# Kernel optimization log

Measured on AMD Instinct MI355X. Metric: run time of the kernel, lower is better.

## Reference

```python
import jax, jax.numpy as jnp
import numpy as np

B, L, D = 1, 2048, 2048
NH, NKV, HD = 32, 8, 64          # heads, kv heads, head_dim = D // NH
THETA = 50000.0
EPS = 1e-5
SCALE = HD ** -0.5


def _rope(x):
    # traditional (interleaved-pair) RoPE; x: (B, H, L, HD)
    hd = x.shape[-1]
    pos = jnp.arange(x.shape[2], dtype=jnp.float32)
    inv = THETA ** (-jnp.arange(0, hd, 2, dtype=jnp.float32) / hd)
    ang = pos[:, None] * inv[None, :]              # (L, HD/2)
    cos, sin = jnp.cos(ang), jnp.sin(ang)
    x1, x2 = x[..., ::2], x[..., 1::2]
    r1 = x1 * cos - x2 * sin
    r2 = x1 * sin + x2 * cos
    return jnp.stack([r1, r2], axis=-1).reshape(x.shape)


def _rmsnorm(x, w):
    return x * jax.lax.rsqrt(jnp.mean(x * x, axis=-1, keepdims=True) + EPS) * w


def setup_inputs() -> dict:
    key = jax.random.key(0)
    ks = jax.random.split(key, 5)
    x = jax.random.normal(ks[0], (B, L, D), dtype=jnp.float32)
    w_qkv = jax.random.normal(ks[1], (NH * HD + 2 * NKV * HD, D), dtype=jnp.float32) * 0.02
    w_out = jax.random.normal(ks[2], (D, D), dtype=jnp.float32) * 0.02
    q_gamma = 1.0 + 0.02 * jax.random.normal(ks[3], (HD,), dtype=jnp.float32)
    k_gamma = 1.0 + 0.02 * jax.random.normal(ks[4], (HD,), dtype=jnp.float32)
    mask = jnp.tril(jnp.ones((L, L), dtype=bool))   # causal
    return {"x": x, "w_qkv": w_qkv, "w_out": w_out,
            "q_gamma": q_gamma, "k_gamma": k_gamma, "mask": mask}


def reference(x, w_qkv, w_out, q_gamma, k_gamma, mask):
    b, l, d = x.shape
    qkv = x @ w_qkv.T                               # fused QKV proj (no bias)
    q, k, v = jnp.split(qkv, [NH * HD, NH * HD + NKV * HD], axis=-1)
    q = q.reshape(b, l, NH, HD).transpose(0, 2, 1, 3)     # (B,NH,L,HD)
    k = k.reshape(b, l, NKV, HD).transpose(0, 2, 1, 3)    # (B,NKV,L,HD)
    v = v.reshape(b, l, NKV, HD).transpose(0, 2, 1, 3)
    q = _rmsnorm(_rope(q), q_gamma)
    k = _rmsnorm(_rope(k), k_gamma)
    g = NH // NKV                                   # GQA group size
    qg = q.reshape(b, NKV, g, l, HD)
    scores = jnp.einsum('bkgqd,bkld->bkgql', qg, k) * SCALE
    scores = jnp.where(mask, scores, -jnp.inf)
    attn = jax.nn.softmax(scores, axis=-1)
    out = jnp.einsum('bkgql,bkld->bkgqd', attn, v)  # (B,NKV,g,L,HD)
    out = out.reshape(b, NH, l, HD).transpose(0, 2, 1, 3).reshape(b, l, d)
    return out @ w_out.T
```

## Files before the change

kernel.cpp:

```cpp
#include <hip/hip_runtime.h>

using bf16   = __bf16;
using bf16x4 = __bf16 __attribute__((ext_vector_type(4)));
using bf16x8 = __bf16 __attribute__((ext_vector_type(8)));
using f32x4  = float __attribute__((ext_vector_type(4)));
using f32x16 = float __attribute__((ext_vector_type(16)));
using u32x2  = unsigned int __attribute__((ext_vector_type(2)));
using u32x4  = unsigned int __attribute__((ext_vector_type(4)));

#define L_SEQ  2048
#define DMODEL 2048
#define NQH    32
#define NKVH   8
#define HDIM   64
#define QKV_N  3072

#define KVF_HSTRIDE (64 * 4 * 64 * 8)

__device__ __forceinline__ void gload_lds16(const void* g, void* lds) {
  __builtin_amdgcn_global_load_lds((__attribute__((address_space(1))) void*)(g),
                                   (__attribute__((address_space(3))) void*)(lds),
                                   16, 0, 0);
}

__device__ __forceinline__ unsigned pack2(float a, float b) {
  union { bf16 h[2]; unsigned u; } x;
  x.h[0] = (bf16)a; x.h[1] = (bf16)b;
  return x.u;
}

__device__ __forceinline__ bf16x8 make_pfrag(float p0, float p1, float p2, float p3,
                                             float p4, float p5, float p6, float p7,
                                             int hi) {
  const unsigned W0 = pack2(p0, p1);
  const unsigned W1 = pack2(p2, p3);
  const unsigned W2 = pack2(p4, p5);
  const unsigned W3 = pack2(p6, p7);
  u32x4 pw;
#if __has_builtin(__builtin_amdgcn_permlane32_swap)
  {
    using i32x2 = int __attribute__((ext_vector_type(2)));
    const i32x2 r02 = __builtin_amdgcn_permlane32_swap((int)W0, (int)W2, false, false);
    const i32x2 r13 = __builtin_amdgcn_permlane32_swap((int)W1, (int)W3, false, false);
    pw = u32x4{ (unsigned)r02[0], (unsigned)r13[0], (unsigned)r02[1], (unsigned)r13[1] };
  }
#else
  {
    const unsigned X0 = (unsigned)__shfl_xor((int)W0, 32);
    const unsigned X1 = (unsigned)__shfl_xor((int)W1, 32);
    const unsigned X2 = (unsigned)__shfl_xor((int)W2, 32);
    const unsigned X3 = (unsigned)__shfl_xor((int)W3, 32);
    pw = u32x4{ hi ? X2 : W0, hi ? X3 : W1, hi ? W2 : X0, hi ? W3 : X1 };
  }
#endif
  return __builtin_bit_cast(bf16x8, pw);
}

__device__ __forceinline__ int chunk_base(int qi) {
  return (qi < 16) ? qi
       : (qi < 32) ? 16 + 2 * (qi - 16)
       : (qi < 48) ? 48 + 3 * (qi - 32)
                   : 96 + 4 * (qi - 48);
}

#define N4_X  (L_SEQ * DMODEL / 4)
#define N4_WQ (QKV_N * DMODEL / 4)
#define N4_WO (DMODEL * DMODEL / 4)
__global__ void cvt3_f32_bf16(const float* __restrict__ x, const float* __restrict__ wq,
                              const float* __restrict__ wo, bf16* __restrict__ xb,
                              bf16* __restrict__ wqb, bf16* __restrict__ wob) {
  const long stride = (long)gridDim.x * blockDim.x;
  const long ntot = N4_X + N4_WQ + N4_WO;
  for (long i = (long)blockIdx.x * blockDim.x + threadIdx.x; i < ntot; i += stride) {
    const float* src; bf16* dst; long j;
    if (i < N4_X)               { src = x;  dst = xb;  j = i; }
    else if (i < N4_X + N4_WQ)  { src = wq; dst = wqb; j = i - N4_X; }
    else                        { src = wo; dst = wob; j = i - N4_X - N4_WQ; }
    const float4 v = reinterpret_cast<const float4*>(src)[j];
    bf16x4 o = { (bf16)v.x, (bf16)v.y, (bf16)v.z, (bf16)v.w };
    reinterpret_cast<bf16x4*>(dst)[j] = o;
  }
}

template <typename OutT>
__global__ __launch_bounds__(128)
void gemm_bt(const bf16* __restrict__ A, const bf16* __restrict__ B,
             OutT* __restrict__ C, int M, int N, int K) {
  __shared__ bf16 As[128 * 64];
  __shared__ bf16 Bs[64 * 64];
  const int tid = threadIdx.x;
  const int w = tid >> 6, l = tid & 63;
  const int lq = l & 15, lg = l >> 4;
  const long m0 = (long)blockIdx.y * 128;
  const long n0 = (long)blockIdx.x * 64;
  const int ks = K / gridDim.z;
  const int kb = blockIdx.z * ks;
  C += (long)blockIdx.z * M * N;

  const int lrow = l >> 3;
  const int scol = ((l & 7) ^ lrow) << 3;

  f32x4 acc[4][4];
#pragma unroll
  for (int i = 0; i < 4; ++i)
#pragma unroll
    for (int j = 0; j < 4; ++j) acc[i][j] = f32x4{0.f, 0.f, 0.f, 0.f};

  for (int k0 = kb; k0 < kb + ks; k0 += 64) {
#pragma unroll
    for (int i = 0; i < 8; ++i) {
      const int r0 = (i * 2 + w) * 8;
      gload_lds16(A + (m0 + r0 + lrow) * (long)K + k0 + scol, &As[r0 * 64]);
    }
#pragma unroll
    for (int i = 0; i < 4; ++i) {
      const int r0 = (i * 2 + w) * 8;
      gload_lds16(B + (n0 + r0 + lrow) * (long)K + k0 + scol, &Bs[r0 * 64]);
    }
    __syncthreads();
#pragma unroll
    for (int kk = 0; kk < 2; ++kk) {
      bf16x8 af[4], bfr[4];
#pragma unroll
      for (int t = 0; t < 4; ++t) {
        const int rowA = w * 64 + t * 16 + lq;
        const int blkA = (kk * 4 + lg) ^ (rowA & 7);
        af[t] = *reinterpret_cast<const bf16x8*>(&As[rowA * 64 + blkA * 8]);
        const int rowB = t * 16 + lq;
        const int blkB = (kk * 4 + lg) ^ (rowB & 7);
        bfr[t] = *reinterpret_cast<const bf16x8*>(&Bs[rowB * 64 + blkB * 8]);
      }
#pragma unroll
      for (int mt = 0; mt < 4; ++mt)
#pragma unroll
        for (int nt = 0; nt < 4; ++nt)
          acc[mt][nt] = __builtin_amdgcn_mfma_f32_16x16x32_bf16(af[mt], bfr[nt], acc[mt][nt], 0, 0, 0);
    }
    __syncthreads();
  }

#pragma unroll
  for (int mt = 0; mt < 4; ++mt)
#pragma unroll
    for (int r = 0; r < 4; ++r) {
      const long row = m0 + w * 64 + mt * 16 + lg * 4 + r;
#pragma unroll
      for (int nt = 0; nt < 4; ++nt) {
        const long col = n0 + nt * 16 + lq;
        C[row * (long)N + col] = (OutT)acc[mt][nt][r];
      }
    }
}

__global__ __launch_bounds__(256)
void rope_rms(const bf16* __restrict__ pA, const bf16* __restrict__ pB,
              const float* __restrict__ qg, const float* __restrict__ kg,
              bf16* __restrict__ qo, bf16* __restrict__ kfr) {
  const int gid = blockIdx.x * 4 + (threadIdx.x >> 6);
  const int lane = threadIdx.x & 63;
  const int pos = gid / 40;
  const int hh = gid % 40;
  const bool isq = hh < 32;
  const int col = isq ? hh * HDIM : NQH * HDIM + (hh - 32) * HDIM;

  const long idx = (long)pos * QKV_N + col + lane;
  float x = (float)pA[idx] + (float)pB[idx];
  float p = __shfl_xor(x, 1);
  const float fi = (float)(lane & ~1) * (1.0f / 64.0f);
  const float inv = powf(50000.0f, -fi);
  const float ang = (float)pos * inv;
  const float sn = sinf(ang), cs = cosf(ang);
  const float r = (lane & 1) ? (p * sn + x * cs) : (x * cs - p * sn);

  float ss = r * r;
#pragma unroll
  for (int off = 1; off < 64; off <<= 1) ss += __shfl_xor(ss, off);
  const float scl = rsqrtf(ss * (1.0f / 64.0f) + 1e-5f);
  const float g = isq ? qg[lane] : kg[lane];
  const float o = r * scl * g;

  if (isq) {
    qo[(long)pos * DMODEL + hh * HDIM + lane] = (bf16)(o * 0.18033688011112042f);
  } else {
    const int kvh = hh - 32;
    const int d = lane;
    const int lp = (pos & 31) + (((d >> 3) & 1) << 5);
    const long kidx = ((((long)kvh * 64 + (pos >> 5)) * 4 + (d >> 4)) * 64 + lp) * 8 + (d & 7);
    kfr[kidx] = (bf16)o;
  }
}

__global__ __launch_bounds__(256)
void repack_v(const bf16* __restrict__ pA, const bf16* __restrict__ pB,
              bf16* __restrict__ vfr) {
  __shared__ bf16 t[32][72];
  const int kvh = blockIdx.x >> 6;
  const int kb = blockIdx.x & 63;
  const int tid = threadIdx.x;

  {
    const int row = tid >> 3;
    const int cc = (tid & 7) * 8;
    const long goff = (long)(kb * 32 + row) * QKV_N + (NQH * HDIM + NKVH * HDIM) + kvh * HDIM + cc;
    const bf16x8 a = *reinterpret_cast<const bf16x8*>(pA + goff);
    const bf16x8 b = *reinterpret_cast<const bf16x8*>(pB + goff);
    bf16x8 s;
#pragma unroll
    for (int e = 0; e < 8; ++e) s[e] = (bf16)((float)a[e] + (float)b[e]);
    *reinterpret_cast<bf16x8*>(&t[row][cc]) = s;
  }
  __syncthreads();

  const int f = tid >> 6, l = tid & 63;
  const int s = f >> 1, dh = f & 1;
  const int hi = l >> 5, l31 = l & 31;
  union { bf16 b[8]; u32x4 u; } o;
#pragma unroll
  for (int e = 0; e < 8; ++e) o.b[e] = t[s * 16 + hi * 8 + e][dh * 32 + l31];
  bf16* od = vfr + (((long)(kvh * 64 + kb) * 4 + f) * 64 + l) * 8;
  *reinterpret_cast<u32x4*>(od) = o.u;
}

__global__ __launch_bounds__(256)
void flash_attn(const bf16* __restrict__ Q, const bf16* __restrict__ Kfr,
                const bf16* __restrict__ Vfr,
                bf16* __restrict__ po, float* __restrict__ pm, float* __restrict__ pl) {
  __shared__ bf16 Ks[2][4096];
  __shared__ bf16 Vs[2][4096];
  const int tid = threadIdx.x;
  const int w = tid >> 6, l = tid & 63;
  const int lane31 = l & 31, hi = l >> 5;
  const int bb = blockIdx.x;
  const int kvh = bb & 7;
  const int g = 159 - (bb >> 3);

  int qi, c;
  if (g < 16)      { qi = g;                  c = 0; }
  else if (g < 48) { qi = 16 + ((g - 16) >> 1); c = (g - 16) & 1; }
  else if (g < 96) { qi = 32 + (g - 48) / 3;    c = (g - 48) % 3; }
  else             { qi = 48 + ((g - 96) >> 2); c = (g - 96) & 3; }

  const int h = kvh * 4 + w;
  const int s0 = c * 16;
  const int s1 = min(qi + 1, s0 + 16);
  const int pidx = h * 160 + g;

  const int q0 = qi * 32;
  const int q_abs = q0 + lane31;
  const int l8 = l * 8;

  const bf16* kfrh = Kfr + (long)kvh * KVF_HSTRIDE;
  const bf16* vfrh = Vfr + (long)kvh * KVF_HSTRIDE;

  const bf16* qrow = Q + (long)q_abs * DMODEL + h * HDIM + hi * 8;
  bf16x8 qf[4];
#pragma unroll
  for (int cc = 0; cc < 4; ++cc) qf[cc] = *reinterpret_cast<const bf16x8*>(qrow + cc * 16);

  f32x16 o0, o1;
#pragma unroll
  for (int r = 0; r < 16; ++r) { o0[r] = 0.f; o1[r] = 0.f; }
  float m = -3.0e38f, lsum = 0.f;

  {
    const long base = (long)s0 * 2048;
    gload_lds16(kfrh + base + tid * 8,        &Ks[0][tid * 8]);
    gload_lds16(kfrh + base + 2048 + tid * 8, &Ks[0][2048 + tid * 8]);
    gload_lds16(vfrh + base + tid * 8,        &Vs[0][tid * 8]);
    gload_lds16(vfrh + base + 2048 + tid * 8, &Vs[0][2048 + tid * 8]);
  }
  __syncthreads();

  int buf = 0;
  int sti = s0;
  for (; sti + 1 < s1; sti += 2) {
    if (sti + 2 < s1) {
      const long base = (long)(sti + 2) * 2048;
      gload_lds16(kfrh + base + tid * 8,        &Ks[buf ^ 1][tid * 8]);
      gload_lds16(kfrh + base + 2048 + tid * 8, &Ks[buf ^ 1][2048 + tid * 8]);
      gload_lds16(vfrh + base + tid * 8,        &Vs[buf ^ 1][tid * 8]);
      gload_lds16(vfrh + base + 2048 + tid * 8, &Vs[buf ^ 1][2048 + tid * 8]);
    }

    f32x16 sa, sb;
#pragma unroll
    for (int r = 0; r < 16; ++r) { sa[r] = 0.f; sb[r] = 0.f; }
#pragma unroll
    for (int cc = 0; cc < 4; ++cc) {
      const bf16x8 ka = *reinterpret_cast<const bf16x8*>(&Ks[buf][cc * 512 + l8]);
      const bf16x8 kb = *reinterpret_cast<const bf16x8*>(&Ks[buf][2048 + cc * 512 + l8]);
      sa = __builtin_amdgcn_mfma_f32_32x32x16_bf16(ka, qf[cc], sa, 0, 0, 0);
      sb = __builtin_amdgcn_mfma_f32_32x32x16_bf16(kb, qf[cc], sb, 0, 0, 0);
    }

    const bf16x8 va0 = *reinterpret_cast<const bf16x8*>(&Vs[buf][l8]);
    const bf16x8 vb0 = *reinterpret_cast<const bf16x8*>(&Vs[buf][512 + l8]);
    const bf16x8 va1 = *reinterpret_cast<const bf16x8*>(&Vs[buf][1024 + l8]);
    const bf16x8 vb1 = *reinterpret_cast<const bf16x8*>(&Vs[buf][1536 + l8]);

    const int kb0a = sti * 32, kb0b = kb0a + 32;
    if (kb0b + 31 > q0) {
#pragma unroll
      for (int r = 0; r < 16; ++r) {
        const int krel = (r & 3) + 8 * (r >> 2) + 4 * hi;
        if (kb0a + krel > q_abs) sa[r] = -3.0e38f;
        if (kb0b + krel > q_abs) sb[r] = -3.0e38f;
      }
    }

    float t[16];
#pragma unroll
    for (int r = 0; r < 16; ++r) t[r] = fmaxf(sa[r], sb[r]);
#pragma unroll
    for (int s = 8; s > 0; s >>= 1)
#pragma unroll
      for (int r = 0; r < 8; ++r) if (r < s) t[r] = fmaxf(t[r], t[r + s]);
    const float mx = fmaxf(t[0], __shfl_xor(t[0], 32));

    if (!__all(mx - m <= 8.0f)) {
      const float mn = fmaxf(m, mx);
      const float al = __builtin_amdgcn_exp2f(m - mn);
      m = mn; lsum *= al;
#pragma unroll
      for (int r = 0; r < 16; ++r) { o0[r] *= al; o1[r] *= al; }
    }
    float rs = 0.f;
#pragma unroll
    for (int r = 0; r < 16; ++r) { sa[r] = __builtin_amdgcn_exp2f(sa[r] - m); rs += sa[r]; }
#pragma unroll
    for (int r = 0; r < 16; ++r) { sb[r] = __builtin_amdgcn_exp2f(sb[r] - m); rs += sb[r]; }
    rs += __shfl_xor(rs, 32);
    lsum += rs;

    {
      const bf16x8 pf0 = make_pfrag(sa[0], sa[1], sa[2], sa[3], sa[4], sa[5], sa[6], sa[7], hi);
      o0 = __builtin_amdgcn_mfma_f32_32x32x16_bf16(va0, pf0, o0, 0, 0, 0);
      o1 = __builtin_amdgcn_mfma_f32_32x32x16_bf16(vb0, pf0, o1, 0, 0, 0);
      const bf16x8 pf1 = make_pfrag(sa[8], sa[9], sa[10], sa[11], sa[12], sa[13], sa[14], sa[15], hi);
      o0 = __builtin_amdgcn_mfma_f32_32x32x16_bf16(va1, pf1, o0, 0, 0, 0);
      o1 = __builtin_amdgcn_mfma_f32_32x32x16_bf16(vb1, pf1, o1, 0, 0, 0);
    }
    {
      const bf16x8 wa0 = *reinterpret_cast<const bf16x8*>(&Vs[buf][2048 + l8]);
      const bf16x8 wb0 = *reinterpret_cast<const bf16x8*>(&Vs[buf][2560 + l8]);
      const bf16x8 wa1 = *reinterpret_cast<const bf16x8*>(&Vs[buf][3072 + l8]);
      const bf16x8 wb1 = *reinterpret_cast<const bf16x8*>(&Vs[buf][3584 + l8]);
      const bf16x8 pf0 = make_pfrag(sb[0], sb[1], sb[2], sb[3], sb[4], sb[5], sb[6], sb[7], hi);
      o0 = __builtin_amdgcn_mfma_f32_32x32x16_bf16(wa0, pf0, o0, 0, 0, 0);
      o1 = __builtin_amdgcn_mfma_f32_32x32x16_bf16(wb0, pf0, o1, 0, 0, 0);
      const bf16x8 pf1 = make_pfrag(sb[8], sb[9], sb[10], sb[11], sb[12], sb[13], sb[14], sb[15], hi);
      o0 = __builtin_amdgcn_mfma_f32_32x32x16_bf16(wa1, pf1, o0, 0, 0, 0);
      o1 = __builtin_amdgcn_mfma_f32_32x32x16_bf16(wb1, pf1, o1, 0, 0, 0);
    }

    __syncthreads();
    buf ^= 1;
  }

  if (sti < s1) {
    const int kb0 = sti * 32;
    f32x16 st;
#pragma unroll
    for (int r = 0; r < 16; ++r) st[r] = 0.f;
#pragma unroll
    for (int cc = 0; cc < 4; ++cc) {
      const bf16x8 ka = *reinterpret_cast<const bf16x8*>(&Ks[buf][cc * 512 + l8]);
      st = __builtin_amdgcn_mfma_f32_32x32x16_bf16(ka, qf[cc], st, 0, 0, 0);
    }
    const bf16x8 va0 = *reinterpret_cast<const bf16x8*>(&Vs[buf][l8]);
    const bf16x8 vb0 = *reinterpret_cast<const bf16x8*>(&Vs[buf][512 + l8]);
    const bf16x8 va1 = *reinterpret_cast<const bf16x8*>(&Vs[buf][1024 + l8]);
    const bf16x8 vb1 = *reinterpret_cast<const bf16x8*>(&Vs[buf][1536 + l8]);

    if (kb0 + 31 > q0) {
#pragma unroll
      for (int r = 0; r < 16; ++r) {
        const int k_abs = kb0 + (r & 3) + 8 * (r >> 2) + 4 * hi;
        if (k_abs > q_abs) st[r] = -3.0e38f;
      }
    }

    float t[8];
#pragma unroll
    for (int r = 0; r < 8; ++r) t[r] = fmaxf(st[r], st[r + 8]);
#pragma unroll
    for (int s = 4; s > 0; s >>= 1)
#pragma unroll
      for (int r = 0; r < 4; ++r) if (r < s) t[r] = fmaxf(t[r], t[r + s]);
    const float mx = fmaxf(t[0], __shfl_xor(t[0], 32));

    if (!__all(mx - m <= 8.0f)) {
      const float mn = fmaxf(m, mx);
      const float al = __builtin_amdgcn_exp2f(m - mn);
      m = mn; lsum *= al;
#pragma unroll
      for (int r = 0; r < 16; ++r) { o0[r] *= al; o1[r] *= al; }
    }
    float rs = 0.f;
#pragma unroll
    for (int r = 0; r < 16; ++r) { st[r] = __builtin_amdgcn_exp2f(st[r] - m); rs += st[r]; }
    rs += __shfl_xor(rs, 32);
    lsum += rs;

    const bf16x8 pf0 = make_pfrag(st[0], st[1], st[2], st[3], st[4], st[5], st[6], st[7], hi);
    o0 = __builtin_amdgcn_mfma_f32_32x32x16_bf16(va0, pf0, o0, 0, 0, 0);
    o1 = __builtin_amdgcn_mfma_f32_32x32x16_bf16(vb0, pf0, o1, 0, 0, 0);
    const bf16x8 pf1 = make_pfrag(st[8], st[9], st[10], st[11], st[12], st[13], st[14], st[15], hi);
    o0 = __builtin_amdgcn_mfma_f32_32x32x16_bf16(va1, pf1, o0, 0, 0, 0);
    o1 = __builtin_amdgcn_mfma_f32_32x32x16_bf16(vb1, pf1, o1, 0, 0, 0);
  }

  bf16* pbase = po + (long)pidx * 2048 + lane31 * 64;
#pragma unroll
  for (int gg = 0; gg < 4; ++gg) {
    const int d0 = 8 * gg + 4 * hi;
    u32x2 s0v = { pack2(o0[4 * gg + 0], o0[4 * gg + 1]),
                  pack2(o0[4 * gg + 2], o0[4 * gg + 3]) };
    u32x2 s1v = { pack2(o1[4 * gg + 0], o1[4 * gg + 1]),
                  pack2(o1[4 * gg + 2], o1[4 * gg + 3]) };
    *reinterpret_cast<u32x2*>(pbase + d0) = s0v;
    *reinterpret_cast<u32x2*>(pbase + 32 + d0) = s1v;
  }
  if (hi == 0) {
    pm[pidx * 32 + lane31] = m;
    pl[pidx * 32 + lane31] = lsum;
  }
}

__global__ __launch_bounds__(256)
void combine_split(const bf16* __restrict__ po, const float* __restrict__ pm,
                   const float* __restrict__ pl, bf16* __restrict__ ao) {
  const int t = blockIdx.x * 2 + (threadIdx.x >> 7);
  const int tid7 = threadIdx.x & 127;
  const int r = tid7 >> 2;
  const int dc = (tid7 & 3) * 16;
  const int h = t >> 6, qi = t & 63;
  const int nc = 1 + (qi >> 4);
  const int p0 = h * 160 + chunk_base(qi);

  float mv0 = -3e38f, mv1 = -3e38f, mv2 = -3e38f, mv3 = -3e38f;
  float lv0 = 0.f, lv1 = 0.f, lv2 = 0.f, lv3 = 0.f;
  mv0 = pm[(p0 + 0) * 32 + r];              lv0 = pl[(p0 + 0) * 32 + r];
  if (nc > 1) { mv1 = pm[(p0 + 1) * 32 + r]; lv1 = pl[(p0 + 1) * 32 + r]; }
  if (nc > 2) { mv2 = pm[(p0 + 2) * 32 + r]; lv2 = pl[(p0 + 2) * 32 + r]; }
  if (nc > 3) { mv3 = pm[(p0 + 3) * 32 + r]; lv3 = pl[(p0 + 3) * 32 + r]; }
  const float M = fmaxf(fmaxf(mv0, mv1), fmaxf(mv2, mv3));
  const float w0 = __builtin_amdgcn_exp2f(mv0 - M);
  const float w1 = (nc > 1) ? __builtin_amdgcn_exp2f(mv1 - M) : 0.f;
  const float w2 = (nc > 2) ? __builtin_amdgcn_exp2f(mv2 - M) : 0.f;
  const float w3 = (nc > 3) ? __builtin_amdgcn_exp2f(mv3 - M) : 0.f;
  const float invL = 1.0f / (lv0 * w0 + lv1 * w1 + lv2 * w2 + lv3 * w3);

  float acc[16];
#pragma unroll
  for (int j = 0; j < 16; ++j) acc[j] = 0.f;

#pragma unroll
  for (int c = 0; c < 4; ++c) {
    if (c < nc) {
      const float fc = ((c == 0) ? w0 : (c == 1) ? w1 : (c == 2) ? w2 : w3) * invL;
      const bf16* src = po + ((long)(p0 + c) * 2048) + r * 64 + dc;
      const bf16x8 a0 = *reinterpret_cast<const bf16x8*>(src);
      const bf16x8 a1 = *reinterpret_cast<const bf16x8*>(src + 8);
#pragma unroll
      for (int j = 0; j < 8; ++j) {
        acc[j]     += (float)a0[j] * fc;
        acc[8 + j] += (float)a1[j] * fc;
      }
    }
  }

  const long q_abs = (long)qi * 32 + r;
  bf16* od = ao + q_abs * DMODEL + h * HDIM + dc;
  union { bf16 b[16]; u32x4 u[2]; } o;
#pragma unroll
  for (int j = 0; j < 16; ++j) o.b[j] = (bf16)acc[j];
  *reinterpret_cast<u32x4*>(od) = o.u[0];
  *reinterpret_cast<u32x4*>(od + 8) = o.u[1];
}

extern "C" void kernel_launch(void* const* d_in, const int* in_sizes, int n_in,
                              void* d_out, int out_size, void* d_ws, size_t ws_size,
                              hipStream_t stream) {
  const float* x       = (const float*)d_in[0];
  const float* w_qkv   = (const float*)d_in[1];
  const float* w_out   = (const float*)d_in[2];
  const float* q_gamma = (const float*)d_in[3];
  const float* k_gamma = (const float*)d_in[4];

  char* ws = (char*)d_ws;
  bf16* xb    = (bf16*)(ws);
  bf16* wqb   = (bf16*)(ws + (8ul  << 20));
  bf16* wob   = (bf16*)(ws + (20ul << 20));
  bf16* qkvpA = (bf16*)(ws + (28ul << 20));
  bf16* qkvpB = (bf16*)(ws + (40ul << 20));
  bf16* qb    = (bf16*)(ws);
  bf16* kfr   = (bf16*)(ws + (8ul  << 20));
  bf16* vfr   = (bf16*)(ws + (10ul << 20));
  bf16* po    = (bf16*)(ws + (28ul << 20));
  float* pm   = (float*)(ws + (48ul << 20));
  float* pl   = (float*)(ws + (49ul << 20));
  bf16* ao    = (bf16*)(ws + (52ul << 20));
  float* out  = (float*)d_out;

  cvt3_f32_bf16<<<2048, 256, 0, stream>>>(x, w_qkv, w_out, xb, wqb, wob);

  gemm_bt<bf16><<<dim3(QKV_N / 64, L_SEQ / 128, 2), 128, 0, stream>>>(xb, wqb, qkvpA, L_SEQ, QKV_N, DMODEL);

  rope_rms<<<(L_SEQ * 40) / 4, 256, 0, stream>>>(qkvpA, qkvpB, q_gamma, k_gamma, qb, kfr);
  repack_v<<<NKVH * (L_SEQ / 32), 256, 0, stream>>>(qkvpA, qkvpB, vfr);

  flash_attn<<<1280, 256, 0, stream>>>(qb, kfr, vfr, po, pm, pl);
  combine_split<<<1024, 256, 0, stream>>>(po, pm, pl, ao);

  gemm_bt<float><<<dim3(DMODEL / 64, L_SEQ / 128, 1), 128, 0, stream>>>(ao, wob, out, L_SEQ, DMODEL, DMODEL);
}
```

Before: 172.0 us.

## Load K/V fragments directly from global into registers, drop LDS staging

```diff
diff --git a/kernel.cpp b/kernel.cpp
--- a/kernel.cpp
+++ b/kernel.cpp
@@ -225,10 +225,7 @@
 void flash_attn(const bf16* __restrict__ Q, const bf16* __restrict__ Kfr,
                 const bf16* __restrict__ Vfr,
                 bf16* __restrict__ po, float* __restrict__ pm, float* __restrict__ pl) {
-  __shared__ bf16 Ks[2][4096];
-  __shared__ bf16 Vs[2][4096];
-  const int tid = threadIdx.x;
-  const int w = tid >> 6, l = tid & 63;
+  const int w = threadIdx.x >> 6, l = threadIdx.x & 63;
   const int lane31 = l & 31, hi = l >> 5;
   const int bb = blockIdx.x;
   const int kvh = bb & 7;
@@ -262,43 +259,52 @@
   for (int r = 0; r < 16; ++r) { o0[r] = 0.f; o1[r] = 0.f; }
   float m = -3.0e38f, lsum = 0.f;
 
+  bf16x8 k0, k1, k2, k3, k4, k5, k6, k7;
   {
-    const long base = (long)s0 * 2048;
-    gload_lds16(kfrh + base + tid * 8,        &Ks[0][tid * 8]);
-    gload_lds16(kfrh + base + 2048 + tid * 8, &Ks[0][2048 + tid * 8]);
-    gload_lds16(vfrh + base + tid * 8,        &Vs[0][tid * 8]);
-    gload_lds16(vfrh + base + 2048 + tid * 8, &Vs[0][2048 + tid * 8]);
-  }
-  __syncthreads();
-
-  int buf = 0;
+    const bf16* kp = kfrh + (long)s0 * 2048 + l8;
+    k0 = *reinterpret_cast<const bf16x8*>(kp);
+    k1 = *reinterpret_cast<const bf16x8*>(kp + 512);
+    k2 = *reinterpret_cast<const bf16x8*>(kp + 1024);
+    k3 = *reinterpret_cast<const bf16x8*>(kp + 1536);
+    k4 = *reinterpret_cast<const bf16x8*>(kp + 2048);
+    k5 = *reinterpret_cast<const bf16x8*>(kp + 2560);
+    k6 = *reinterpret_cast<const bf16x8*>(kp + 3072);
+    k7 = *reinterpret_cast<const bf16x8*>(kp + 3584);
+  }
+
   int sti = s0;
   for (; sti + 1 < s1; sti += 2) {
-    if (sti + 2 < s1) {
-      const long base = (long)(sti + 2) * 2048;
-      gload_lds16(kfrh + base + tid * 8,        &Ks[buf ^ 1][tid * 8]);
-      gload_lds16(kfrh + base + 2048 + tid * 8, &Ks[buf ^ 1][2048 + tid * 8]);
-      gload_lds16(vfrh + base + tid * 8,        &Vs[buf ^ 1][tid * 8]);
-      gload_lds16(vfrh + base + 2048 + tid * 8, &Vs[buf ^ 1][2048 + tid * 8]);
-    }
+    const int kb0a = sti * 32, kb0b = kb0a + 32;
 
     f32x16 sa, sb;
 #pragma unroll
     for (int r = 0; r < 16; ++r) { sa[r] = 0.f; sb[r] = 0.f; }
-#pragma unroll
-    for (int cc = 0; cc < 4; ++cc) {
-      const bf16x8 ka = *reinterpret_cast<const bf16x8*>(&Ks[buf][cc * 512 + l8]);
-      const bf16x8 kb = *reinterpret_cast<const bf16x8*>(&Ks[buf][2048 + cc * 512 + l8]);
-      sa = __builtin_amdgcn_mfma_f32_32x32x16_bf16(ka, qf[cc], sa, 0, 0, 0);
-      sb = __builtin_amdgcn_mfma_f32_32x32x16_bf16(kb, qf[cc], sb, 0, 0, 0);
-    }
-
-    const bf16x8 va0 = *reinterpret_cast<const bf16x8*>(&Vs[buf][l8]);
-    const bf16x8 vb0 = *reinterpret_cast<const bf16x8*>(&Vs[buf][512 + l8]);
-    const bf16x8 va1 = *reinterpret_cast<const bf16x8*>(&Vs[buf][1024 + l8]);
-    const bf16x8 vb1 = *reinterpret_cast<const bf16x8*>(&Vs[buf][1536 + l8]);
-
-    const int kb0a = sti * 32, kb0b = kb0a + 32;
+    sa = __builtin_amdgcn_mfma_f32_32x32x16_bf16(k0, qf[0], sa, 0, 0, 0);
+    sb = __builtin_amdgcn_mfma_f32_32x32x16_bf16(k4, qf[0], sb, 0, 0, 0);
+    sa = __builtin_amdgcn_mfma_f32_32x32x16_bf16(k1, qf[1], sa, 0, 0, 0);
+    sb = __builtin_amdgcn_mfma_f32_32x32x16_bf16(k5, qf[1], sb, 0, 0, 0);
+    sa = __builtin_amdgcn_mfma_f32_32x32x16_bf16(k2, qf[2], sa, 0, 0, 0);
+    sb = __builtin_amdgcn_mfma_f32_32x32x16_bf16(k6, qf[2], sb, 0, 0, 0);
+    sa = __builtin_amdgcn_mfma_f32_32x32x16_bf16(k3, qf[3], sa, 0, 0, 0);
+    sb = __builtin_amdgcn_mfma_f32_32x32x16_bf16(k7, qf[3], sb, 0, 0, 0);
+
+    const bf16* vp = vfrh + (long)sti * 2048 + l8;
+    const bf16x8 va0 = *reinterpret_cast<const bf16x8*>(vp);
+    const bf16x8 vb0 = *reinterpret_cast<const bf16x8*>(vp + 512);
+    const bf16x8 va1 = *reinterpret_cast<const bf16x8*>(vp + 1024);
+    const bf16x8 vb1 = *reinterpret_cast<const bf16x8*>(vp + 1536);
+
+    const long knoff = (sti + 2 < s1) ? (long)(sti + 2) * 2048 : (long)s0 * 2048;
+    const bf16* kp = kfrh + knoff + l8;
+    const bf16x8 n0 = *reinterpret_cast<const bf16x8*>(kp);
+    const bf16x8 n1 = *reinterpret_cast<const bf16x8*>(kp + 512);
+    const bf16x8 n2 = *reinterpret_cast<const bf16x8*>(kp + 1024);
+    const bf16x8 n3 = *reinterpret_cast<const bf16x8*>(kp + 1536);
+    const bf16x8 n4 = *reinterpret_cast<const bf16x8*>(kp + 2048);
+    const bf16x8 n5 = *reinterpret_cast<const bf16x8*>(kp + 2560);
+    const bf16x8 n6 = *reinterpret_cast<const bf16x8*>(kp + 3072);
+    const bf16x8 n7 = *reinterpret_cast<const bf16x8*>(kp + 3584);
+
     if (kb0b + 31 > q0) {
 #pragma unroll
       for (int r = 0; r < 16; ++r) {
@@ -331,6 +337,11 @@
     for (int r = 0; r < 16; ++r) { sb[r] = __builtin_amdgcn_exp2f(sb[r] - m); rs += sb[r]; }
     rs += __shfl_xor(rs, 32);
     lsum += rs;
+
+    const bf16x8 wa0 = *reinterpret_cast<const bf16x8*>(vp + 2048);
+    const bf16x8 wb0 = *reinterpret_cast<const bf16x8*>(vp + 2560);
+    const bf16x8 wa1 = *reinterpret_cast<const bf16x8*>(vp + 3072);
+    const bf16x8 wb1 = *reinterpret_cast<const bf16x8*>(vp + 3584);
 
     {
       const bf16x8 pf0 = make_pfrag(sa[0], sa[1], sa[2], sa[3], sa[4], sa[5], sa[6], sa[7], hi);
@@ -341,10 +352,6 @@
       o1 = __builtin_amdgcn_mfma_f32_32x32x16_bf16(vb1, pf1, o1, 0, 0, 0);
     }
     {
-      const bf16x8 wa0 = *reinterpret_cast<const bf16x8*>(&Vs[buf][2048 + l8]);
-      const bf16x8 wb0 = *reinterpret_cast<const bf16x8*>(&Vs[buf][2560 + l8]);
-      const bf16x8 wa1 = *reinterpret_cast<const bf16x8*>(&Vs[buf][3072 + l8]);
-      const bf16x8 wb1 = *reinterpret_cast<const bf16x8*>(&Vs[buf][3584 + l8]);
       const bf16x8 pf0 = make_pfrag(sb[0], sb[1], sb[2], sb[3], sb[4], sb[5], sb[6], sb[7], hi);
       o0 = __builtin_amdgcn_mfma_f32_32x32x16_bf16(wa0, pf0, o0, 0, 0, 0);
       o1 = __builtin_amdgcn_mfma_f32_32x32x16_bf16(wb0, pf0, o1, 0, 0, 0);
@@ -353,8 +360,8 @@
       o1 = __builtin_amdgcn_mfma_f32_32x32x16_bf16(wb1, pf1, o1, 0, 0, 0);
     }
 
-    __syncthreads();
-    buf ^= 1;
+    k0 = n0; k1 = n1; k2 = n2; k3 = n3;
+    k4 = n4; k5 = n5; k6 = n6; k7 = n7;
   }
 
   if (sti < s1) {
@@ -362,15 +369,16 @@
     f32x16 st;
 #pragma unroll
     for (int r = 0; r < 16; ++r) st[r] = 0.f;
-#pragma unroll
-    for (int cc = 0; cc < 4; ++cc) {
-      const bf16x8 ka = *reinterpret_cast<const bf16x8*>(&Ks[buf][cc * 512 + l8]);
-      st = __builtin_amdgcn_mfma_f32_32x32x16_bf16(ka, qf[cc], st, 0, 0, 0);
-    }
-    const bf16x8 va0 = *reinterpret_cast<const bf16x8*>(&Vs[buf][l8]);
-    const bf16x8 vb0 = *reinterpret_cast<const bf16x8*>(&Vs[buf][512 + l8]);
-    const bf16x8 va1 = *reinterpret_cast<const bf16x8*>(&Vs[buf][1024 + l8]);
-    const bf16x8 vb1 = *reinterpret_cast<const bf16x8*>(&Vs[buf][1536 + l8]);
+    st = __builtin_amdgcn_mfma_f32_32x32x16_bf16(k0, qf[0], st, 0, 0, 0);
+    st = __builtin_amdgcn_mfma_f32_32x32x16_bf16(k1, qf[1], st, 0, 0, 0);
+    st = __builtin_amdgcn_mfma_f32_32x32x16_bf16(k2, qf[2], st, 0, 0, 0);
+    st = __builtin_amdgcn_mfma_f32_32x32x16_bf16(k3, qf[3], st, 0, 0, 0);
+
+    const bf16* vp = vfrh + (long)sti * 2048 + l8;
+    const bf16x8 va0 = *reinterpret_cast<const bf16x8*>(vp);
+    const bf16x8 vb0 = *reinterpret_cast<const bf16x8*>(vp + 512);
+    const bf16x8 va1 = *reinterpret_cast<const bf16x8*>(vp + 1024);
+    const bf16x8 vb1 = *reinterpret_cast<const bf16x8*>(vp + 1536);
 
     if (kb0 + 31 > q0) {
 #pragma unroll
```

Result: no change. 168.7 us (-1.9%).
